# Performance work log

Hardware: AMD Instinct MI355X
Metric: run time of the kernel (lower is better)

Reference implementation:

```python
import jax, jax.numpy as jnp
from jax import lax
import numpy as np

U = 512          # LSTMOutUnits
NL = 3           # stacked LSTM cells
EMB = 300
VOCAB = 50000
LABELS = 7
BN_EPS = 1e-3    # keras BatchNormalization default epsilon


def _lstm_cell(x, h, c, W, Uw, b):
    # keras LSTMCell: gates ordered i, f, g(c), o; activation=softsign, recurrent_activation=sigmoid
    z = x @ W + h @ Uw + b                      # [B, 4U]
    i, f, g, o = jnp.split(z, 4, axis=-1)
    c = jax.nn.sigmoid(f) * c + jax.nn.sigmoid(i) * jax.nn.soft_sign(g)
    h = jax.nn.sigmoid(o) * jax.nn.soft_sign(c)
    return h, c


def _run_stack(x_tbd, Ws, Us, bs):
    # x_tbd: [T, B, D]; returns final hidden state of top cell: [B, U]
    B = x_tbd.shape[1]
    init = tuple((jnp.zeros((B, U), x_tbd.dtype), jnp.zeros((B, U), x_tbd.dtype)) for _ in range(NL))

    def step(carry, x):
        new = []
        inp = x
        for (h, c), W, Uw, b in zip(carry, Ws, Us, bs):
            h, c = _lstm_cell(inp, h, c, W, Uw, b)
            new.append((h, c))
            inp = h
        return tuple(new), None

    carry, _ = lax.scan(step, init, x_tbd)
    return carry[-1][0]


def setup_inputs() -> dict:
    key = jax.random.key(0)
    ks = iter(jax.random.split(key, 40))
    d = {}
    d['ids'] = jax.random.randint(next(ks), (128, 128), 0, VOCAB, dtype=jnp.int32)
    d['emb'] = jax.random.normal(next(ks), (VOCAB, EMB), jnp.float32)
    for pre in ('f', 'b'):
        for l in range(NL):
            din = EMB if l == 0 else U
            d[f'{pre}W{l}'] = jax.random.normal(next(ks), (din, 4 * U), jnp.float32) * 0.05
            d[f'{pre}U{l}'] = jax.random.normal(next(ks), (U, 4 * U), jnp.float32) * 0.05
            d[f'{pre}b{l}'] = jnp.zeros((4 * U,), jnp.float32)
    d['d0_W'] = jax.random.normal(next(ks), (U, U // 2), jnp.float32) * 0.05
    d['d0_b'] = jnp.zeros((U // 2,), jnp.float32)
    d['bn_gamma'] = jnp.ones((U // 2,), jnp.float32)
    d['bn_beta'] = jnp.zeros((U // 2,), jnp.float32)
    d['bn_mean'] = jnp.zeros((U // 2,), jnp.float32)
    d['bn_var'] = jnp.ones((U // 2,), jnp.float32)
    d['prelu_alpha'] = jnp.full((U // 2,), 0.25, jnp.float32)
    d['d1_W'] = jax.random.normal(next(ks), (U // 2, LABELS), jnp.float32) * 0.05
    d['d1_b'] = jnp.zeros((LABELS,), jnp.float32)
    return d


def reference(ids, emb,
              fW0, fU0, fb0, fW1, fU1, fb1, fW2, fU2, fb2,
              bW0, bU0, bb0, bW1, bU1, bb1, bW2, bU2, bb2,
              d0_W, d0_b, bn_gamma, bn_beta, bn_mean, bn_var,
              prelu_alpha, d1_W, d1_b):
    x = lax.stop_gradient(jnp.take(emb, ids, axis=0))      # [B, T, EMB]
    x = jnp.transpose(x, (1, 0, 2))                        # [T, B, EMB]
    fwd = _run_stack(x, (fW0, fW1, fW2), (fU0, fU1, fU2), (fb0, fb1, fb2))
    bwd = _run_stack(x[::-1], (bW0, bW1, bW2), (bU0, bU1, bU2), (bb0, bb1, bb2))
    add = 0.5 * (fwd + bwd)                                # [B, U]
    h = add @ d0_W + d0_b                                  # [B, U//2]
    h = (h - bn_mean) * lax.rsqrt(bn_var + BN_EPS) * bn_gamma + bn_beta
    h = jnp.where(h > 0, h, prelu_alpha * h)               # PReLU
    logits = h @ d1_W + d1_b                               # [B, LABELS]
    return jax.nn.softmax(logits, axis=-1)
```

## Files before the change

### kernel.cpp

```cpp
#include <hip/hip_runtime.h>
#include <hip/hip_bf16.h>
#include <math.h>

#define TT   128
#define BB   128
#define UU   512
#define EMBD 300
#define EMBP 320
#define NBLK 192
#define DBLK 96
#define NTHR 256
#define BSTR 1056

using bf16x8 = __attribute__((ext_vector_type(8))) short;
using f32x4  = __attribute__((ext_vector_type(4))) float;

#define NEED_WS 111681536ull
static void* g_pool = nullptr;
__attribute__((constructor)) static void alloc_pool() {
    if (hipMalloc(&g_pool, 120ull * 1024ull * 1024ull) != hipSuccess) g_pool = nullptr;
}

__device__ __forceinline__ float b2f(unsigned short u) {
    union { unsigned int i; float f; } v; v.i = ((unsigned int)u) << 16; return v.f;
}
__device__ __forceinline__ unsigned short f2b(float f) {
    union { unsigned int i; float f; } v; v.f = f;
    unsigned int i = v.i;
    return (unsigned short)((i + 0x7fffu + ((i >> 16) & 1u)) >> 16);
}
__device__ __forceinline__ unsigned short ld_bf(const void* p, size_t i, int f32) {
    return f32 ? f2b(((const float*)p)[i]) : ((const unsigned short*)p)[i];
}
__device__ __forceinline__ float ld_f(const void* p, size_t i, int f32) {
    return f32 ? ((const float*)p)[i] : b2f(((const unsigned short*)p)[i]);
}
__device__ __forceinline__ float clampz(float x) {
    return fminf(fmaxf(x, -60.0f), 60.0f);
}
__device__ __forceinline__ float sigm(float x)  { return 1.0f / (1.0f + __expf(-x)); }
__device__ __forceinline__ float ssign(float x) { return x / (1.0f + fabsf(x)); }

__device__ __forceinline__ int detect_f32(const void* emb) {
    const unsigned int* w = (const unsigned int*)emb;
    int cnt = 0;
    #pragma unroll
    for (int i = 0; i < 64; ++i) {
        unsigned int e = (w[i] >> 23) & 0xFFu;
        cnt += (e >= 96u && e <= 159u) ? 1 : 0;
    }
    return cnt >= 48;
}

struct P {
    const int* ids;
    const void* emb;
    const void* Wm[2][3];
    const void* Um[2][3];
    const void* bm[2][3];
    const void *d0W, *d0b;
    const void *bn_gamma, *bn_beta, *bn_mean, *bn_var;
    const void *alpha, *d1W, *d1b;
    unsigned short* X;
    unsigned short* H;
    float* hf;
    unsigned int* flags;
    unsigned int* epoch;
    float* out;
};

#define EPOFF 64

__device__ __forceinline__ unsigned int ald(const unsigned int* a) {
    return __hip_atomic_load(a, __ATOMIC_RELAXED, __HIP_MEMORY_SCOPE_AGENT);
}
__device__ __forceinline__ void ast(unsigned int* a, unsigned int v) {
    __hip_atomic_store(a, v, __ATOMIC_RELAXED, __HIP_MEMORY_SCOPE_AGENT);
}

__device__ __forceinline__ void gsync_fence(unsigned int* flags, unsigned int gen) {
    __syncthreads();
    if (threadIdx.x == 0) {
        __threadfence();
        ast(&flags[blockIdx.x], gen);
    }
    if (threadIdx.x < 64) {
        const int i = threadIdx.x;
        for (;;) {
            bool ok = true;
            #pragma unroll
            for (int j = 0; j < NBLK / 64; ++j)
                ok = ok && (ald(&flags[i + j * 64]) >= gen);
            if (__all(ok)) break;
            __builtin_amdgcn_s_sleep(1);
        }
        __threadfence();
    }
    __syncthreads();
}

__device__ __forceinline__ void gsync_dir(P& p, int dirbase, int eidx, int isagg, unsigned int gen) {
    __syncthreads();
    if (threadIdx.x == 0)
        ast(&p.flags[blockIdx.x], gen);
    if (isagg && threadIdx.x < 64) {
        const unsigned int* f = p.flags + dirbase + threadIdx.x;
        const bool two = (threadIdx.x < DBLK - 64);
        for (;;) {
            bool ok = (ald(f) >= gen) && (!two || (ald(f + 64) >= gen));
            if (__all(ok)) break;
            __builtin_amdgcn_s_sleep(1);
        }
        if (threadIdx.x == 0)
            ast(&p.epoch[eidx], gen);
    }
    if (threadIdx.x < 64) {
        const unsigned int* e = &p.epoch[eidx];
        while (ald(e) < gen) __builtin_amdgcn_s_sleep(1);
    }
    __syncthreads();
}

__device__ __forceinline__ void gsync_all(P& p, int dirbase, int eidx, int isagg, unsigned int gen) {
    __syncthreads();
    if (threadIdx.x == 0)
        ast(&p.flags[blockIdx.x], gen);
    if (isagg && threadIdx.x < 64) {
        const unsigned int* f = p.flags + dirbase + threadIdx.x;
        const bool two = (threadIdx.x < DBLK - 64);
        for (;;) {
            bool ok = (ald(f) >= gen) && (!two || (ald(f + 64) >= gen));
            if (__all(ok)) break;
            __builtin_amdgcn_s_sleep(1);
        }
        if (threadIdx.x == 0)
            ast(&p.epoch[eidx], gen);
    }
    if (threadIdx.x < 64) {
        while (!((ald(&p.epoch[0]) >= gen) && (ald(&p.epoch[EPOFF]) >= gen)))
            __builtin_amdgcn_s_sleep(1);
    }
    __syncthreads();
}

template<int K1T, int BOFF>
__device__ __forceinline__ void mfma_part(
    const unsigned short* __restrict__ a0p,
    const unsigned short* __restrict__ a1p,
    const unsigned short* __restrict__ bp,
    f32x4 (&acc)[4][2])
{
    #pragma unroll 4
    for (int kt = 0; kt < K1T; kt += 32) {
        bf16x8 av0 = *(const bf16x8*)(a0p + kt);
        bf16x8 av1 = *(const bf16x8*)(a1p + kt);
        #pragma unroll
        for (int ct = 0; ct < 4; ++ct) {
            bf16x8 bv = *(const bf16x8*)(bp + (size_t)ct * 16 * BSTR + BOFF + kt);
            acc[ct][0] = __builtin_amdgcn_mfma_f32_16x16x32_bf16(av0, bv, acc[ct][0], 0, 0, 0);
            acc[ct][1] = __builtin_amdgcn_mfma_f32_16x16x32_bf16(av1, bv, acc[ct][1], 0, 0, 0);
        }
    }
}

__global__ __launch_bounds__(NTHR, 1) void bilstm_persistent(P p) {
    const int blk = blockIdx.x;
    const int tid = threadIdx.x;

    const int f32 = detect_f32(p.emb);
    unsigned int gen = 0;

    __shared__ __align__(16) unsigned short Bt[64][BSTR];
    __shared__ __align__(16) float zbuf[4][32][17];
    __shared__ float hact[256];
    __shared__ float lgts[8];

    for (int row = blk; row < TT * BB; row += NBLK) {
        int t = row >> 7, b = row & 127;
        int id = p.ids[b * TT + t];
        unsigned short* xr = p.X + (size_t)row * EMBP;
        for (int k2 = tid; k2 < EMBP; k2 += NTHR)
            xr[k2] = (k2 < EMBD) ? ld_bf(p.emb, (size_t)id * EMBD + k2, f32)
                                 : (unsigned short)0;
    }
    gsync_fence(p.flags, ++gen);

    const int dir     = (blk >= DBLK) ? 1 : 0;
    const int rb      = blk - dir * DBLK;
    const int layer   = rb >> 5;
    const int dirbase = dir * DBLK;
    const int eidx    = dir * EPOFF;
    const int isagg   = (rb == 0);
    const int j0      = (rb & 31) * 16;

    const int wv   = tid >> 6;
    const int lane = tid & 63;
    const int l15  = lane & 15;
    const int quad = lane >> 4;

    const int rr   = lane & 31;
    const int jA   = (lane >> 5) * 2;

    const int r0   = wv * 32 + l15;
    const int r1   = r0 + 16;
    const int ko   = quad * 8;

    float cS[4][2];
    #pragma unroll
    for (int ct = 0; ct < 4; ++ct) { cS[ct][0] = 0.0f; cS[ct][1] = 0.0f; }

    const size_t seq = (size_t)TT * BB * UU;

    const int KW   = (layer == 0) ? EMBD : UU;
    const int K1   = (layer == 0) ? EMBP : UU;
    const int Ktot = K1 + UU;
    const void* Wmat = p.Wm[dir][layer];
    const void* Umat = p.Um[dir][layer];
    const void* bias = p.bm[dir][layer];
    {
        int n = tid >> 2, ks = tid & 3;
        int wcol = ((n >> 2) & 3) * UU + j0 + (n >> 4) * 4 + (n & 3);
        for (int k2 = ks; k2 < Ktot; k2 += 4) {
            unsigned short v;
            if (k2 < KW)      v = ld_bf(Wmat, (size_t)k2 * 2048 + wcol, f32);
            else if (k2 < K1) v = 0;
            else              v = ld_bf(Umat, (size_t)(k2 - K1) * 2048 + wcol, f32);
            Bt[n][k2] = v;
        }
    }
    float bz[4][4][2];
    #pragma unroll
    for (int ct = 0; ct < 4; ++ct)
        #pragma unroll
        for (int g = 0; g < 4; ++g) {
            bz[ct][g][0] = ld_f(bias, g * UU + j0 + ct * 4 + jA,     f32);
            bz[ct][g][1] = ld_f(bias, g * UU + j0 + ct * 4 + jA + 1, f32);
        }
    __syncthreads();

    unsigned short*       Hl  = p.H + (size_t)(layer * 2 + dir) * seq;
    const unsigned short* Hin = (layer > 0) ? (p.H + (size_t)((layer - 1) * 2 + dir) * seq) : nullptr;

    const unsigned short* bp = &Bt[l15][ko];
    float* zb = &zbuf[wv][0][0];

    for (int s = 0; s < TT + 2; ++s) {
        const int t = s - layer;
        if (t >= 0 && t < TT) {
            const unsigned short* A2 = (t > 0) ? (Hl + (size_t)(t - 1) * BB * UU) : nullptr;

            f32x4 acc[4][2];
            #pragma unroll
            for (int ct = 0; ct < 4; ++ct) {
                acc[ct][0] = f32x4{0.f, 0.f, 0.f, 0.f};
                acc[ct][1] = f32x4{0.f, 0.f, 0.f, 0.f};
            }

            if (layer == 0) {
                int tx = dir ? (TT - 1 - t) : t;
                const unsigned short* A1 = p.X + (size_t)tx * BB * EMBP;
                mfma_part<EMBP, 0>(A1 + (size_t)r0 * EMBP + ko, A1 + (size_t)r1 * EMBP + ko, bp, acc);
                if (A2)
                    mfma_part<UU, EMBP>(A2 + (size_t)r0 * UU + ko, A2 + (size_t)r1 * UU + ko, bp, acc);
            } else {
                const unsigned short* A1 = Hin + (size_t)t * BB * UU;
                mfma_part<UU, 0>(A1 + (size_t)r0 * UU + ko, A1 + (size_t)r1 * UU + ko, bp, acc);
                if (A2)
                    mfma_part<UU, UU>(A2 + (size_t)r0 * UU + ko, A2 + (size_t)r1 * UU + ko, bp, acc);
            }

            #pragma unroll
            for (int ct = 0; ct < 4; ++ct) {
                #pragma unroll
                for (int r = 0; r < 4; ++r) {
                    zb[(quad * 4 + r) * 17 + l15]        = acc[ct][0][r];
                    zb[(16 + quad * 4 + r) * 17 + l15]   = acc[ct][1][r];
                }
                float ziA = clampz(zb[rr * 17 +  0 + jA] + bz[ct][0][0]);
                float zfA = clampz(zb[rr * 17 +  4 + jA] + bz[ct][1][0]);
                float zgA = clampz(zb[rr * 17 +  8 + jA] + bz[ct][2][0]);
                float zoA = clampz(zb[rr * 17 + 12 + jA] + bz[ct][3][0]);
                float ziB = clampz(zb[rr * 17 +  1 + jA] + bz[ct][0][1]);
                float zfB = clampz(zb[rr * 17 +  5 + jA] + bz[ct][1][1]);
                float zgB = clampz(zb[rr * 17 +  9 + jA] + bz[ct][2][1]);
                float zoB = clampz(zb[rr * 17 + 13 + jA] + bz[ct][3][1]);
                float cpA = (t == 0) ? 0.0f : cS[ct][0];
                float cpB = (t == 0) ? 0.0f : cS[ct][1];
                float cnA = sigm(zfA) * cpA + sigm(ziA) * ssign(zgA);
                float cnB = sigm(zfB) * cpB + sigm(ziB) * ssign(zgB);
                cS[ct][0] = cnA; cS[ct][1] = cnB;
                float hA = sigm(zoA) * ssign(cnA);
                float hB = sigm(zoB) * ssign(cnB);
                const int R = wv * 32 + rr;
                const int col = j0 + ct * 4 + jA;
                unsigned int pk = (unsigned int)f2b(hA) | ((unsigned int)f2b(hB) << 16);
                __hip_atomic_store((unsigned int*)&Hl[(size_t)t * BB * UU + (size_t)R * UU + col],
                                   pk, __ATOMIC_RELAXED, __HIP_MEMORY_SCOPE_AGENT);
                if (layer == 2 && t == TT - 1) {
                    size_t o = (size_t)dir * BB * UU + (size_t)R * UU + col;
                    __hip_atomic_store(&p.hf[o],     hA, __ATOMIC_RELAXED, __HIP_MEMORY_SCOPE_AGENT);
                    __hip_atomic_store(&p.hf[o + 1], hB, __ATOMIC_RELAXED, __HIP_MEMORY_SCOPE_AGENT);
                }
            }
        }
        gsync_dir(p, dirbase, eidx, isagg, ++gen);
    }

    gsync_all(p, dirbase, eidx, isagg, ++gen);

    if (blk < BB) {
        const int b = blk;
        const float* h0 = p.hf + (size_t)b * UU;
        const float* h1 = p.hf + (size_t)BB * UU + (size_t)b * UU;
        float acc = ld_f(p.d0b, tid, f32);
        #pragma unroll 8
        for (int k = 0; k < UU; ++k) {
            float a = 0.5f * (h0[k] + h1[k]);
            acc = fmaf(a, ld_f(p.d0W, (size_t)k * 256 + tid, f32), acc);
        }
        acc = fminf(fmaxf(acc, -1e6f), 1e6f);
        float x = (acc - ld_f(p.bn_mean, tid, f32))
                  * rsqrtf(fmaxf(ld_f(p.bn_var, tid, f32), 0.0f) + 1e-3f)
                  * ld_f(p.bn_gamma, tid, f32) + ld_f(p.bn_beta, tid, f32);
        float al = ld_f(p.alpha, tid, f32);
        hact[tid] = (x > 0.f) ? x : al * x;
        __syncthreads();
        if (tid < 7) {
            float s = ld_f(p.d1b, tid, f32);
            #pragma unroll 8
            for (int k = 0; k < 256; ++k)
                s = fmaf(hact[k], ld_f(p.d1W, k * 7 + tid, f32), s);
            lgts[tid] = fminf(fmaxf(s, -1e6f), 1e6f);
        }
        __syncthreads();
        if (tid == 0) {
            float mx = lgts[0];
            for (int j = 1; j < 7; ++j) mx = fmaxf(mx, lgts[j]);
            float ex[7]; float sum = 0.f;
            for (int j = 0; j < 7; ++j) { ex[j] = __expf(lgts[j] - mx); sum += ex[j]; }
            float inv = 1.0f / sum;
            for (int j = 0; j < 7; ++j) p.out[b * 7 + j] = ex[j] * inv;
        }
    }
}

extern "C" void kernel_launch(void* const* d_in, const int* in_sizes, int n_in,
                              void* d_out, int out_size, void* d_ws, size_t ws_size,
                              hipStream_t stream) {
    (void)in_sizes; (void)n_in; (void)out_size;

    P p;
    p.ids = (const int*)d_in[0];
    p.emb = d_in[1];
    for (int l = 0; l < 3; ++l) {
        p.Wm[0][l] = d_in[2 + l * 3];
        p.Um[0][l] = d_in[3 + l * 3];
        p.bm[0][l] = d_in[4 + l * 3];
        p.Wm[1][l] = d_in[11 + l * 3];
        p.Um[1][l] = d_in[12 + l * 3];
        p.bm[1][l] = d_in[13 + l * 3];
    }
    p.d0W      = d_in[20];
    p.d0b      = d_in[21];
    p.bn_gamma = d_in[22];
    p.bn_beta  = d_in[23];
    p.bn_mean  = d_in[24];
    p.bn_var   = d_in[25];
    p.alpha    = d_in[26];
    p.d1W      = d_in[27];
    p.d1b      = d_in[28];

    char* base = (ws_size >= NEED_WS || g_pool == nullptr) ? (char*)d_ws : (char*)g_pool;
    const size_t OFF_X  = 8192;
    const size_t OFF_H  = OFF_X + (size_t)TT * BB * EMBP * 2;
    const size_t OFF_HF = OFF_H + (size_t)3 * 2 * TT * BB * UU * 2;
    p.flags = (unsigned int*)base;
    p.epoch = (unsigned int*)(base + 4096);
    p.X     = (unsigned short*)(base + OFF_X);
    p.H     = (unsigned short*)(base + OFF_H);
    p.hf    = (float*)(base + OFF_HF);
    p.out   = (float*)d_out;

    hipMemsetAsync(base, 0, 8192, stream);
    hipLaunchKernelGGL(bilstm_persistent, dim3(NBLK), dim3(NTHR), 0, stream, p);
}
```

Before: 1.867 ms.

## Double block threads so each wave handles sixteen batch rows

Raises the block size from 256 to 512 threads, so eight waves each compute a 16-row batch slice instead of four waves with 32 rows. This halves each wave's MFMA chain and accumulator count per timestep and splits the gate epilogue across lanes, aiming to cut per-step latency in the latency-bound recurrence. The LDS weight row stride is also narrowed to 1032, which changes bank mapping. More waves share the same LDS B tiles, raising LDS read pressure and possible bank conflicts, and the final dense layer is now guarded to 256 threads.

```diff
diff --git a/kernel.cpp b/kernel.cpp
--- a/kernel.cpp
+++ b/kernel.cpp
@@ -9,8 +9,8 @@
 #define EMBP 320
 #define NBLK 192
 #define DBLK 96
-#define NTHR 256
-#define BSTR 1056
+#define NTHR 512
+#define BSTR 1032
 
 using bf16x8 = __attribute__((ext_vector_type(8))) short;
 using f32x4  = __attribute__((ext_vector_type(4))) float;
@@ -146,19 +146,16 @@
 template<int K1T, int BOFF>
 __device__ __forceinline__ void mfma_part(
     const unsigned short* __restrict__ a0p,
-    const unsigned short* __restrict__ a1p,
     const unsigned short* __restrict__ bp,
-    f32x4 (&acc)[4][2])
+    f32x4 (&acc)[4])
 {
     #pragma unroll 4
     for (int kt = 0; kt < K1T; kt += 32) {
-        bf16x8 av0 = *(const bf16x8*)(a0p + kt);
-        bf16x8 av1 = *(const bf16x8*)(a1p + kt);
+        bf16x8 av = *(const bf16x8*)(a0p + kt);
         #pragma unroll
         for (int ct = 0; ct < 4; ++ct) {
             bf16x8 bv = *(const bf16x8*)(bp + (size_t)ct * 16 * BSTR + BOFF + kt);
-            acc[ct][0] = __builtin_amdgcn_mfma_f32_16x16x32_bf16(av0, bv, acc[ct][0], 0, 0, 0);
-            acc[ct][1] = __builtin_amdgcn_mfma_f32_16x16x32_bf16(av1, bv, acc[ct][1], 0, 0, 0);
+            acc[ct] = __builtin_amdgcn_mfma_f32_16x16x32_bf16(av, bv, acc[ct], 0, 0, 0);
         }
     }
 }
@@ -171,7 +168,7 @@
     unsigned int gen = 0;
 
     __shared__ __align__(16) unsigned short Bt[64][BSTR];
-    __shared__ __align__(16) float zbuf[4][32][17];
+    __shared__ __align__(16) float zbuf[8][2][16][17];
     __shared__ float hact[256];
     __shared__ float lgts[8];
 
@@ -198,16 +195,15 @@
     const int l15  = lane & 15;
     const int quad = lane >> 4;
 
-    const int rr   = lane & 31;
-    const int jA   = (lane >> 5) * 2;
-
-    const int r0   = wv * 32 + l15;
-    const int r1   = r0 + 16;
+    const int row16 = lane & 15;
+    const int jp    = (lane >> 4) & 1;
+    const int ch    = lane >> 5;
+
+    const int r0   = wv * 16 + l15;
     const int ko   = quad * 8;
 
-    float cS[4][2];
-    #pragma unroll
-    for (int ct = 0; ct < 4; ++ct) { cS[ct][0] = 0.0f; cS[ct][1] = 0.0f; }
+    float cS[2][2];
+    cS[0][0] = cS[0][1] = cS[1][0] = cS[1][1] = 0.0f;
 
     const size_t seq = (size_t)TT * BB * UU;
 
@@ -218,9 +214,9 @@
     const void* Umat = p.Um[dir][layer];
     const void* bias = p.bm[dir][layer];
     {
-        int n = tid >> 2, ks = tid & 3;
+        int n = tid >> 3, ks = tid & 7;
         int wcol = ((n >> 2) & 3) * UU + j0 + (n >> 4) * 4 + (n & 3);
-        for (int k2 = ks; k2 < Ktot; k2 += 4) {
+        for (int k2 = ks; k2 < Ktot; k2 += 8) {
             unsigned short v;
             if (k2 < KW)      v = ld_bf(Wmat, (size_t)k2 * 2048 + wcol, f32);
             else if (k2 < K1) v = 0;
@@ -228,71 +224,73 @@
             Bt[n][k2] = v;
         }
     }
-    float bz[4][4][2];
+    float bz[2][4][2];
     #pragma unroll
-    for (int ct = 0; ct < 4; ++ct)
+    for (int pp = 0; pp < 2; ++pp) {
+        const int cb = j0 + (2 * pp + ch) * 4 + 2 * jp;
         #pragma unroll
         for (int g = 0; g < 4; ++g) {
-            bz[ct][g][0] = ld_f(bias, g * UU + j0 + ct * 4 + jA,     f32);
-            bz[ct][g][1] = ld_f(bias, g * UU + j0 + ct * 4 + jA + 1, f32);
-        }
+            bz[pp][g][0] = ld_f(bias, g * UU + cb,     f32);
+            bz[pp][g][1] = ld_f(bias, g * UU + cb + 1, f32);
+        }
+    }
     __syncthreads();
 
     unsigned short*       Hl  = p.H + (size_t)(layer * 2 + dir) * seq;
     const unsigned short* Hin = (layer > 0) ? (p.H + (size_t)((layer - 1) * 2 + dir) * seq) : nullptr;
 
     const unsigned short* bp = &Bt[l15][ko];
-    float* zb = &zbuf[wv][0][0];
+    float* zbw = &zbuf[wv][0][0][0];
 
     for (int s = 0; s < TT + 2; ++s) {
         const int t = s - layer;
         if (t >= 0 && t < TT) {
             const unsigned short* A2 = (t > 0) ? (Hl + (size_t)(t - 1) * BB * UU) : nullptr;
 
-            f32x4 acc[4][2];
+            f32x4 acc[4];
             #pragma unroll
-            for (int ct = 0; ct < 4; ++ct) {
-                acc[ct][0] = f32x4{0.f, 0.f, 0.f, 0.f};
-                acc[ct][1] = f32x4{0.f, 0.f, 0.f, 0.f};
-            }
+            for (int ct = 0; ct < 4; ++ct) acc[ct] = f32x4{0.f, 0.f, 0.f, 0.f};
 
             if (layer == 0) {
                 int tx = dir ? (TT - 1 - t) : t;
                 const unsigned short* A1 = p.X + (size_t)tx * BB * EMBP;
-                mfma_part<EMBP, 0>(A1 + (size_t)r0 * EMBP + ko, A1 + (size_t)r1 * EMBP + ko, bp, acc);
+                mfma_part<EMBP, 0>(A1 + (size_t)r0 * EMBP + ko, bp, acc);
                 if (A2)
-                    mfma_part<UU, EMBP>(A2 + (size_t)r0 * UU + ko, A2 + (size_t)r1 * UU + ko, bp, acc);
+                    mfma_part<UU, EMBP>(A2 + (size_t)r0 * UU + ko, bp, acc);
             } else {
                 const unsigned short* A1 = Hin + (size_t)t * BB * UU;
-                mfma_part<UU, 0>(A1 + (size_t)r0 * UU + ko, A1 + (size_t)r1 * UU + ko, bp, acc);
+                mfma_part<UU, 0>(A1 + (size_t)r0 * UU + ko, bp, acc);
                 if (A2)
-                    mfma_part<UU, UU>(A2 + (size_t)r0 * UU + ko, A2 + (size_t)r1 * UU + ko, bp, acc);
+                    mfma_part<UU, UU>(A2 + (size_t)r0 * UU + ko, bp, acc);
             }
 
             #pragma unroll
-            for (int ct = 0; ct < 4; ++ct) {
+            for (int pp = 0; pp < 2; ++pp) {
                 #pragma unroll
-                for (int r = 0; r < 4; ++r) {
-                    zb[(quad * 4 + r) * 17 + l15]        = acc[ct][0][r];
-                    zb[(16 + quad * 4 + r) * 17 + l15]   = acc[ct][1][r];
+                for (int cth = 0; cth < 2; ++cth) {
+                    const int ct = pp * 2 + cth;
+                    #pragma unroll
+                    for (int r = 0; r < 4; ++r)
+                        zbw[cth * 272 + (quad * 4 + r) * 17 + l15] = acc[ct][r];
                 }
-                float ziA = clampz(zb[rr * 17 +  0 + jA] + bz[ct][0][0]);
-                float zfA = clampz(zb[rr * 17 +  4 + jA] + bz[ct][1][0]);
-                float zgA = clampz(zb[rr * 17 +  8 + jA] + bz[ct][2][0]);
-                float zoA = clampz(zb[rr * 17 + 12 + jA] + bz[ct][3][0]);
-                float ziB = clampz(zb[rr * 17 +  1 + jA] + bz[ct][0][1]);
-                float zfB = clampz(zb[rr * 17 +  5 + jA] + bz[ct][1][1]);
-                float zgB = clampz(zb[rr * 17 +  9 + jA] + bz[ct][2][1]);
-                float zoB = clampz(zb[rr * 17 + 13 + jA] + bz[ct][3][1]);
-                float cpA = (t == 0) ? 0.0f : cS[ct][0];
-                float cpB = (t == 0) ? 0.0f : cS[ct][1];
+                const int zb0 = ch * 272 + row16 * 17 + 2 * jp;
+                float ziA = clampz(zbw[zb0 +  0] + bz[pp][0][0]);
+                float zfA = clampz(zbw[zb0 +  4] + bz[pp][1][0]);
+                float zgA = clampz(zbw[zb0 +  8] + bz[pp][2][0]);
+                float zoA = clampz(zbw[zb0 + 12] + bz[pp][3][0]);
+                float ziB = clampz(zbw[zb0 +  1] + bz[pp][0][1]);
+                float zfB = clampz(zbw[zb0 +  5] + bz[pp][1][1]);
+                float zgB = clampz(zbw[zb0 +  9] + bz[pp][2][1]);
+                float zoB = clampz(zbw[zb0 + 13] + bz[pp][3][1]);
+                float cpA = (t == 0) ? 0.0f : cS[pp][0];
+                float cpB = (t == 0) ? 0.0f : cS[pp][1];
                 float cnA = sigm(zfA) * cpA + sigm(ziA) * ssign(zgA);
                 float cnB = sigm(zfB) * cpB + sigm(ziB) * ssign(zgB);
-                cS[ct][0] = cnA; cS[ct][1] = cnB;
+                cS[pp][0] = cnA; cS[pp][1] = cnB;
                 float hA = sigm(zoA) * ssign(cnA);
                 float hB = sigm(zoB) * ssign(cnB);
-                const int R = wv * 32 + rr;
-                const int col = j0 + ct * 4 + jA;
+                const int R   = wv * 16 + row16;
+                const int col = j0 + (2 * pp + ch) * 4 + 2 * jp;
                 unsigned int pk = (unsigned int)f2b(hA) | ((unsigned int)f2b(hB) << 16);
                 __hip_atomic_store((unsigned int*)&Hl[(size_t)t * BB * UU + (size_t)R * UU + col],
                                    pk, __ATOMIC_RELAXED, __HIP_MEMORY_SCOPE_AGENT);
@@ -310,20 +308,22 @@
 
     if (blk < BB) {
         const int b = blk;
-        const float* h0 = p.hf + (size_t)b * UU;
-        const float* h1 = p.hf + (size_t)BB * UU + (size_t)b * UU;
-        float acc = ld_f(p.d0b, tid, f32);
-        #pragma unroll 8
-        for (int k = 0; k < UU; ++k) {
-            float a = 0.5f * (h0[k] + h1[k]);
-            acc = fmaf(a, ld_f(p.d0W, (size_t)k * 256 + tid, f32), acc);
-        }
-        acc = fminf(fmaxf(acc, -1e6f), 1e6f);
-        float x = (acc - ld_f(p.bn_mean, tid, f32))
-                  * rsqrtf(fmaxf(ld_f(p.bn_var, tid, f32), 0.0f) + 1e-3f)
-                  * ld_f(p.bn_gamma, tid, f32) + ld_f(p.bn_beta, tid, f32);
-        float al = ld_f(p.alpha, tid, f32);
-        hact[tid] = (x > 0.f) ? x : al * x;
+        if (tid < 256) {
+            const float* h0 = p.hf + (size_t)b * UU;
+            const float* h1 = p.hf + (size_t)BB * UU + (size_t)b * UU;
+            float acc = ld_f(p.d0b, tid, f32);
+            #pragma unroll 8
+            for (int k = 0; k < UU; ++k) {
+                float a = 0.5f * (h0[k] + h1[k]);
+                acc = fmaf(a, ld_f(p.d0W, (size_t)k * 256 + tid, f32), acc);
+            }
+            acc = fminf(fmaxf(acc, -1e6f), 1e6f);
+            float x = (acc - ld_f(p.bn_mean, tid, f32))
+                      * rsqrtf(fmaxf(ld_f(p.bn_var, tid, f32), 0.0f) + 1e-3f)
+                      * ld_f(p.bn_gamma, tid, f32) + ld_f(p.bn_beta, tid, f32);
+            float al = ld_f(p.alpha, tid, f32);
+            hact[tid] = (x > 0.f) ? x : al * x;
+        }
         __syncthreads();
         if (tid < 7) {
             float s = ld_f(p.d1b, tid, f32);
```

Result: faster. 1.674 ms (-10.4%).
